# Performance work log

Hardware: AMD Instinct MI355X
Metric: run time of the kernel (lower is better)

The kernel has to match this reference:

```python
import jax, jax.numpy as jnp
import numpy as np

H = 1024
S = 32768

def setup_inputs() -> dict:
    key = jax.random.key(0)
    k1, k2, k3, k4 = jax.random.split(key, 4)
    hidden = jax.random.normal(k1, (H,), dtype=jnp.float32)
    encoder_outputs = jax.random.normal(k2, (S, H), dtype=jnp.float32)
    # nn.Linear(H, H) params, scaled like torch default init
    bound = 1.0 / np.sqrt(H)
    W = jax.random.uniform(k3, (H, H), minval=-bound, maxval=bound, dtype=jnp.float32)
    b = jax.random.uniform(k4, (H,), minval=-bound, maxval=bound, dtype=jnp.float32)
    return {"hidden": hidden, "encoder_outputs": encoder_outputs, "W": W, "b": b}

def reference(hidden, encoder_outputs, W, b):
    # method == 'general': energy_i = hidden . (W @ e_i + b)
    # batched over all timesteps in one matmul instead of a Python loop
    proj = jnp.einsum('sh,dh->sd', encoder_outputs, W) + b  # [S, H]
    energies = proj @ hidden                                 # [S]
    attn = jax.nn.softmax(energies)                          # softmax over seq_len
    return attn[None, None, :]                               # [1, 1, S]
```

## Files before the change

kernel.cpp:

```cpp
#include <hip/hip_runtime.h>
#include <math.h>

#define H 1024
#define S 32768


__global__ __launch_bounds__(256) void compute_v(const float* __restrict__ W,
                                                 const float* __restrict__ hidden,
                                                 float* __restrict__ v) {
    int h = blockIdx.x * 256 + threadIdx.x;
    int d0 = blockIdx.y * 16;
    float acc = 0.f;
#pragma unroll
    for (int j = 0; j < 16; ++j) {
        int d = d0 + j;
        acc += W[(size_t)d * H + h] * hidden[d];
    }
    atomicAdd(&v[h], acc);
}

__global__ __launch_bounds__(256) void energies_kernel(const float* __restrict__ enc,
                                                       const float* __restrict__ v,
                                                       float* __restrict__ energies,
                                                       float* __restrict__ pmax,
                                                       float* __restrict__ psum) {
    const int lane = threadIdx.x & 63;
    const int wave = threadIdx.x >> 6;

    const float4* v4 = (const float4*)v;
    float4 va = v4[lane];
    float4 vb = v4[64 + lane];
    float4 vc = v4[128 + lane];
    float4 vd = v4[192 + lane];

    const int s0 = blockIdx.x * 16 + wave * 4;
    const float4* base = (const float4*)(enc + (size_t)s0 * H);

    float dot[4];
#pragma unroll
    for (int r = 0; r < 4; ++r) {
        const float4* row = base + r * (H / 4);
        float4 a = row[lane];
        float4 b = row[64 + lane];
        float4 c = row[128 + lane];
        float4 d = row[192 + lane];
        float t = a.x * va.x + a.y * va.y + a.z * va.z + a.w * va.w;
        t += b.x * vb.x + b.y * vb.y + b.z * vb.z + b.w * vb.w;
        t += c.x * vc.x + c.y * vc.y + c.z * vc.z + c.w * vc.w;
        t += d.x * vd.x + d.y * vd.y + d.z * vd.z + d.w * vd.w;
        dot[r] = t;
    }

#pragma unroll
    for (int off = 32; off > 0; off >>= 1) {
#pragma unroll
        for (int r = 0; r < 4; ++r) dot[r] += __shfl_xor(dot[r], off, 64);
    }

    if (lane == 0) {
        float4 e = make_float4(dot[0], dot[1], dot[2], dot[3]);
        *(float4*)(energies + s0) = e;
    }

    float m = fmaxf(fmaxf(dot[0], dot[1]), fmaxf(dot[2], dot[3]));
    float sum = __expf(dot[0] - m) + __expf(dot[1] - m) +
                __expf(dot[2] - m) + __expf(dot[3] - m);

    __shared__ float wm[4], wsum[4];
    if (lane == 0) { wm[wave] = m; wsum[wave] = sum; }
    __syncthreads();
    if (threadIdx.x == 0) {
        float M = wm[0], Sm = wsum[0];
#pragma unroll
        for (int w = 1; w < 4; ++w) {
            float Mn = fmaxf(M, wm[w]);
            Sm = Sm * __expf(M - Mn) + wsum[w] * __expf(wm[w] - Mn);
            M = Mn;
        }
        pmax[blockIdx.x] = M;
        psum[blockIdx.x] = Sm;
    }
}

__global__ __launch_bounds__(1024) void combine(const float* __restrict__ pmax,
                                                const float* __restrict__ psum,
                                                float* __restrict__ MS) {
    const int tid = threadIdx.x;
    const int lane = tid & 63;
    const int wave = tid >> 6;

    float m1 = pmax[tid], s1 = psum[tid];
    float m2 = pmax[tid + 1024], s2 = psum[tid + 1024];
    float M = fmaxf(m1, m2);
    float Sv = s1 * __expf(m1 - M) + s2 * __expf(m2 - M);

#pragma unroll
    for (int off = 32; off > 0; off >>= 1) {
        float Mo = __shfl_xor(M, off, 64);
        float So = __shfl_xor(Sv, off, 64);
        float Mn = fmaxf(M, Mo);
        Sv = Sv * __expf(M - Mn) + So * __expf(Mo - Mn);
        M = Mn;
    }

    __shared__ float sm[16], ss[16];
    if (lane == 0) { sm[wave] = M; ss[wave] = Sv; }
    __syncthreads();
    if (wave == 0) {
        float Mv = (lane < 16) ? sm[lane] : -INFINITY;
        float Sw = (lane < 16) ? ss[lane] : 0.f;
#pragma unroll
        for (int off = 8; off > 0; off >>= 1) {
            float Mo = __shfl_xor(Mv, off, 64);
            float So = __shfl_xor(Sw, off, 64);
            float Mn = fmaxf(Mv, Mo);
            Sw = Sw * __expf(Mv - Mn) + So * __expf(Mo - Mn);
            Mv = Mn;
        }
        if (lane == 0) {
            MS[0] = Mv;
            MS[1] = 1.0f / Sw;
        }
    }
}

__global__ __launch_bounds__(256) void finalize(float* __restrict__ out,
                                                const float* __restrict__ MS) {
    int i = blockIdx.x * 256 + threadIdx.x;
    float M = MS[0];
    float inv = MS[1];
    float4 e = ((const float4*)out)[i];
    float4 o;
    o.x = __expf(e.x - M) * inv;
    o.y = __expf(e.y - M) * inv;
    o.z = __expf(e.z - M) * inv;
    o.w = __expf(e.w - M) * inv;
    ((float4*)out)[i] = o;
}

extern "C" void kernel_launch(void* const* d_in, const int* in_sizes, int n_in,
                              void* d_out, int out_size, void* d_ws, size_t ws_size,
                              hipStream_t stream) {
    const float* hidden = (const float*)d_in[0];
    const float* enc    = (const float*)d_in[1];
    const float* W      = (const float*)d_in[2];

    float* ws   = (float*)d_ws;
    float* v    = ws;
    float* pmax = ws + 1024;
    float* psum = ws + 3072;
    float* MS   = ws + 5120;
    float* out  = (float*)d_out;

    hipMemsetAsync(v, 0, H * sizeof(float), stream);
    compute_v<<<dim3(4, 64), 256, 0, stream>>>(W, hidden, v);
    energies_kernel<<<S / 16, 256, 0, stream>>>(enc, v, out, pmax, psum);
    combine<<<1, 1024, 0, stream>>>(pmax, psum, MS);
    finalize<<<S / 4 / 256, 256, 0, stream>>>(out, MS);
}
```

Measured before the change: 203.7 us.

## Fuse softmax combine and normalize into energies kernel via last-block counter

Result: slower. 310.4 us (+52.4%).

```diff
diff --git a/kernel.cpp b/kernel.cpp
--- a/kernel.cpp
+++ b/kernel.cpp
@@ -3,6 +3,7 @@
 
 #define H 1024
 #define S 32768
+#define NBLK (S / 16)
 
 
 __global__ __launch_bounds__(256) void compute_v(const float* __restrict__ W,
@@ -19,13 +20,22 @@
     atomicAdd(&v[h], acc);
 }
 
-__global__ __launch_bounds__(256) void energies_kernel(const float* __restrict__ enc,
-                                                       const float* __restrict__ v,
-                                                       float* __restrict__ energies,
-                                                       float* __restrict__ pmax,
-                                                       float* __restrict__ psum) {
+#define MERGE(M, Sv, Mo, So)                                   \
+    do {                                                       \
+        float _mn = fmaxf((M), (Mo));                          \
+        (Sv) = (Sv) * __expf((M) - _mn) + (So) * __expf((Mo) - _mn); \
+        (M) = _mn;                                             \
+    } while (0)
+
+__global__ __launch_bounds__(256) void energies_fused(const float* __restrict__ enc,
+                                                      const float* __restrict__ v,
+                                                      float* __restrict__ out,
+                                                      float* __restrict__ pmax,
+                                                      float* __restrict__ psum,
+                                                      unsigned* __restrict__ counter) {
     const int lane = threadIdx.x & 63;
     const int wave = threadIdx.x >> 6;
+    const int tid = threadIdx.x;
 
     const float4* v4 = (const float4*)v;
     float4 va = v4[lane];
@@ -59,7 +69,7 @@
 
     if (lane == 0) {
         float4 e = make_float4(dot[0], dot[1], dot[2], dot[3]);
-        *(float4*)(energies + s0) = e;
+        *(float4*)(out + s0) = e;
     }
 
     float m = fmaxf(fmaxf(dot[0], dot[1]), fmaxf(dot[2], dot[3]));
@@ -67,75 +77,65 @@
                 __expf(dot[2] - m) + __expf(dot[3] - m);
 
     __shared__ float wm[4], wsum[4];
+    __shared__ int sLast;
     if (lane == 0) { wm[wave] = m; wsum[wave] = sum; }
     __syncthreads();
-    if (threadIdx.x == 0) {
+    if (tid == 0) {
         float M = wm[0], Sm = wsum[0];
 #pragma unroll
-        for (int w = 1; w < 4; ++w) {
-            float Mn = fmaxf(M, wm[w]);
-            Sm = Sm * __expf(M - Mn) + wsum[w] * __expf(wm[w] - Mn);
-            M = Mn;
-        }
+        for (int w = 1; w < 4; ++w) MERGE(M, Sm, wm[w], wsum[w]);
         pmax[blockIdx.x] = M;
         psum[blockIdx.x] = Sm;
+        __threadfence();
+        unsigned old = atomicAdd(counter, 1u);
+        sLast = (old == NBLK - 1);
     }
-}
+    __syncthreads();
+    if (!sLast) return;
 
-__global__ __launch_bounds__(1024) void combine(const float* __restrict__ pmax,
-                                                const float* __restrict__ psum,
-                                                float* __restrict__ MS) {
-    const int tid = threadIdx.x;
-    const int lane = tid & 63;
-    const int wave = tid >> 6;
+    __threadfence();
 
-    float m1 = pmax[tid], s1 = psum[tid];
-    float m2 = pmax[tid + 1024], s2 = psum[tid + 1024];
-    float M = fmaxf(m1, m2);
-    float Sv = s1 * __expf(m1 - M) + s2 * __expf(m2 - M);
+    const float4* pm4 = (const float4*)pmax;
+    const float4* ps4 = (const float4*)psum;
+    float4 ma = pm4[tid * 2 + 0], mb = pm4[tid * 2 + 1];
+    float4 sa = ps4[tid * 2 + 0], sb = ps4[tid * 2 + 1];
+    float M = ma.x, Sv = sa.x;
+    MERGE(M, Sv, ma.y, sa.y);
+    MERGE(M, Sv, ma.z, sa.z);
+    MERGE(M, Sv, ma.w, sa.w);
+    MERGE(M, Sv, mb.x, sb.x);
+    MERGE(M, Sv, mb.y, sb.y);
+    MERGE(M, Sv, mb.z, sb.z);
+    MERGE(M, Sv, mb.w, sb.w);
 
 #pragma unroll
     for (int off = 32; off > 0; off >>= 1) {
         float Mo = __shfl_xor(M, off, 64);
         float So = __shfl_xor(Sv, off, 64);
-        float Mn = fmaxf(M, Mo);
-        Sv = Sv * __expf(M - Mn) + So * __expf(Mo - Mn);
-        M = Mn;
+        MERGE(M, Sv, Mo, So);
     }
 
-    __shared__ float sm[16], ss[16];
-    if (lane == 0) { sm[wave] = M; ss[wave] = Sv; }
+    __shared__ float fm[4], fs[4];
+    if (lane == 0) { fm[wave] = M; fs[wave] = Sv; }
     __syncthreads();
-    if (wave == 0) {
-        float Mv = (lane < 16) ? sm[lane] : -INFINITY;
-        float Sw = (lane < 16) ? ss[lane] : 0.f;
-#pragma unroll
-        for (int off = 8; off > 0; off >>= 1) {
-            float Mo = __shfl_xor(Mv, off, 64);
-            float So = __shfl_xor(Sw, off, 64);
-            float Mn = fmaxf(Mv, Mo);
-            Sw = Sw * __expf(Mv - Mn) + So * __expf(Mo - Mn);
-            Mv = Mn;
-        }
-        if (lane == 0) {
-            MS[0] = Mv;
-            MS[1] = 1.0f / Sw;
-        }
+    float Mf = fm[0], Sf = fs[0];
+    MERGE(Mf, Sf, fm[1], fs[1]);
+    MERGE(Mf, Sf, fm[2], fs[2]);
+    MERGE(Mf, Sf, fm[3], fs[3]);
+    float inv = 1.0f / Sf;
+
+    float4* out4 = (float4*)out;
+#pragma unroll 8
+    for (int k = 0; k < 32; ++k) {
+        int idx = k * 256 + tid;
+        float4 e = out4[idx];
+        float4 o;
+        o.x = __expf(e.x - Mf) * inv;
+        o.y = __expf(e.y - Mf) * inv;
+        o.z = __expf(e.z - Mf) * inv;
+        o.w = __expf(e.w - Mf) * inv;
+        out4[idx] = o;
     }
-}
-
-__global__ __launch_bounds__(256) void finalize(float* __restrict__ out,
-                                                const float* __restrict__ MS) {
-    int i = blockIdx.x * 256 + threadIdx.x;
-    float M = MS[0];
-    float inv = MS[1];
-    float4 e = ((const float4*)out)[i];
-    float4 o;
-    o.x = __expf(e.x - M) * inv;
-    o.y = __expf(e.y - M) * inv;
-    o.z = __expf(e.z - M) * inv;
-    o.w = __expf(e.w - M) * inv;
-    ((float4*)out)[i] = o;
 }
 
 extern "C" void kernel_launch(void* const* d_in, const int* in_sizes, int n_in,
@@ -145,16 +145,14 @@
     const float* enc    = (const float*)d_in[1];
     const float* W      = (const float*)d_in[2];
 
-    float* ws   = (float*)d_ws;
-    float* v    = ws;
-    float* pmax = ws + 1024;
-    float* psum = ws + 3072;
-    float* MS   = ws + 5120;
-    float* out  = (float*)d_out;
+    float* ws = (float*)d_ws;
+    float* v = ws;
+    unsigned* counter = (unsigned*)(ws + 1024);
+    float* pmax = ws + 1088;
+    float* psum = ws + 3136;
+    float* out = (float*)d_out;
 
-    hipMemsetAsync(v, 0, H * sizeof(float), stream);
+    hipMemsetAsync(v, 0, (H + 64) * sizeof(float), stream);
     compute_v<<<dim3(4, 64), 256, 0, stream>>>(W, hidden, v);
-    energies_kernel<<<S / 16, 256, 0, stream>>>(enc, v, out, pmax, psum);
-    combine<<<1, 1024, 0, stream>>>(pmax, psum, MS);
-    finalize<<<S / 4 / 256, 256, 0, stream>>>(out, MS);
+    energies_fused<<<NBLK, 256, 0, stream>>>(enc, v, out, pmax, psum, counter);
 }
```
